# Performance work log

Hardware: AMD Instinct MI355X
Metric: run time of the kernel (lower is better)

Reference implementation:

```python
import jax, jax.numpy as jnp
import numpy as np

B, H, W, K, A = 4096, 32, 32, 20, 4


def setup_inputs() -> dict:
    key = jax.random.key(0)
    k_wall, k_agent, k_goal, k_phi, k_l1, k_l2 = jax.random.split(key, 6)
    # obs channels: 0 = wall/feature map (random), 1 = one-hot agent pos, 2 = one-hot goal pos
    walls = jax.random.uniform(k_wall, (B, H, W), dtype=jnp.float32)
    agent_idx = jax.random.randint(k_agent, (B,), 0, H * W)
    goal_idx = jax.random.randint(k_goal, (B,), 0, H * W)
    agent = jax.nn.one_hot(agent_idx, H * W, dtype=jnp.float32).reshape(B, H, W)
    goal = jax.nn.one_hot(goal_idx, H * W, dtype=jnp.float32).reshape(B, H, W)
    obs = jnp.stack([walls, agent, goal], axis=-1)  # (B,H,W,3)
    obs_flat = obs.reshape(B, H * W * 3)
    din = H * W * 3
    return {
        "obs_flat": obs_flat,
        "Phi_w": jax.random.normal(k_phi, (din, 2 * H * W), dtype=jnp.float32) * 0.02,
        "Phi_b": jnp.zeros((2 * H * W,), jnp.float32),
        "L1_w": jax.random.normal(k_l1, (36, 16), dtype=jnp.float32) * 0.1,
        "L1_b": jnp.zeros((16,), jnp.float32),
        "L2_w": jax.random.normal(k_l2, (16, A), dtype=jnp.float32) * 0.1,
        "L2_b": jnp.zeros((A,), jnp.float32),
    }


def _mvprop(r, p):
    # K-step value propagation: V <- max(V, r + p*(best 4-neighbor V - r))
    # p = sigmoid(...) >= 0, so max over the 4 shifted nv values equals nv of the max shift.
    def body(V, _):
        pv = jnp.pad(V, ((0, 0), (1, 1), (1, 1)))
        nbr = jnp.maximum(
            jnp.maximum(pv[:, :-2, 1:-1], pv[:, 2:, 1:-1]),   # up, down
            jnp.maximum(pv[:, 1:-1, :-2], pv[:, 1:-1, 2:]),   # left, right
        )
        return jnp.maximum(V, r + p * (nbr - r)), None
    V, _ = jax.lax.scan(body, r, None, length=K)
    return V


def reference(obs_flat, Phi_w, Phi_b, L1_w, L1_b, L2_w, L2_b):
    b = obs_flat.shape[0]
    obs = obs_flat.reshape(b, H, W, 3)
    phi = jax.nn.sigmoid(obs_flat @ Phi_w + Phi_b).reshape(b, H, W, 2)
    r, p = phi[..., 0], phi[..., 1]
    V = _mvprop(r, p)  # (b,H,W)
    obs_val = jnp.concatenate([obs, V[..., None]], axis=-1)  # (b,H,W,4)
    padded = jnp.pad(obs_val, ((0, 0), (1, 1), (1, 1), (0, 0)))
    # agent position: exactly one nonzero in channel 1 per sample -> argmax
    idx = jnp.argmax(obs[..., 1].reshape(b, -1), axis=1)
    pi, pj = idx // W, idx % W
    # 3x3 neighborhood around agent in padded grid (start = pos+1-1 = pos)
    def slice_one(ov, i, j):
        return jax.lax.dynamic_slice(ov, (i, j, 0), (3, 3, 4))
    sel = jax.vmap(slice_one)(padded, pi, pj)  # (b,3,3,4)
    h = jax.nn.relu(sel.reshape(b, 36) @ L1_w + L1_b)
    logit = h @ L2_w + L2_b
    return logit
```

## Files before the change

kernel.cpp:

```cpp
#include <hip/hip_runtime.h>
#include <hip/hip_fp16.h>

#define BATCH 4096
#define HH 32
#define WW 32
#define KPROP 20
#define NACT 4
#define DIN 3072
#define DPHI 2048
#define HWC 1024
#define KC 1024

typedef _Float16 h8_t __attribute__((ext_vector_type(8)));
typedef _Float16 h4_t __attribute__((ext_vector_type(4)));
typedef float f32x4 __attribute__((ext_vector_type(4)));

__device__ inline void load_lds16(const _Float16* g, _Float16* l) {
    __builtin_amdgcn_global_load_lds(
        (const __attribute__((address_space(1))) void*)g,
        (__attribute__((address_space(3))) void*)l, 16, 0, 0);
}

__device__ inline float sigmoidf(float x) { return 1.0f / (1.0f + __expf(-x)); }

__device__ inline float dpp_shr1(float x) {
    return __int_as_float(__builtin_amdgcn_update_dpp(
        0, __float_as_int(x), 0x111, 0xF, 0xF, true));
}
__device__ inline float dpp_shl1(float x) {
    return __int_as_float(__builtin_amdgcn_update_dpp(
        0, __float_as_int(x), 0x101, 0xF, 0xF, true));
}

__global__ __launch_bounds__(256) void prep_fused_kernel(
    const float* __restrict__ obs,
    const float* __restrict__ Phi_w,
    _Float16* __restrict__ W16,
    _Float16* __restrict__ PwT,
    _Float16* __restrict__ Pag,
    int* __restrict__ aidx, int* __restrict__ gidx)
{
    __shared__ float tile[32][33];
    if (blockIdx.x < BATCH) {
        const int t = blockIdx.x * 256 + threadIdx.x;
        const int b = t >> 8;
        const int c0 = (t & 255) * 4;
        const float* src = obs + (size_t)b * DIN + 3 * c0;
        const float4 f0 = *(const float4*)(src);
        const float4 f1 = *(const float4*)(src + 4);
        const float4 f2 = *(const float4*)(src + 8);
        h4_t w;
        w[0] = (_Float16)f0.x; w[1] = (_Float16)f0.w;
        w[2] = (_Float16)f1.z; w[3] = (_Float16)f2.y;
        *(h4_t*)(W16 + (size_t)b * KC + c0) = w;
        if (f0.y > 0.5f) aidx[b] = c0;
        if (f1.x > 0.5f) aidx[b] = c0 + 1;
        if (f1.w > 0.5f) aidx[b] = c0 + 2;
        if (f2.z > 0.5f) aidx[b] = c0 + 3;
        if (f0.z > 0.5f) gidx[b] = c0;
        if (f1.y > 0.5f) gidx[b] = c0 + 1;
        if (f2.x > 0.5f) gidx[b] = c0 + 2;
        if (f2.w > 0.5f) gidx[b] = c0 + 3;
    } else {
        const int bid = blockIdx.x - BATCH;
        const int ni = bid & 63;
        const int ci = bid >> 6;
        const int tx = threadIdx.x & 31;
        const int ty = threadIdx.x >> 5;
        #pragma unroll
        for (int s = 0; s < 4; s++) {
            const int r = ty + 8 * s;
            const int c = ci * 32 + r;
            const int n = ni * 32 + tx;
            tile[r][tx] = Phi_w[(size_t)(3 * c) * DPHI + n];
            Pag[(size_t)c * DPHI + n]         = (_Float16)Phi_w[(size_t)(3 * c + 1) * DPHI + n];
            Pag[(size_t)(HWC + c) * DPHI + n] = (_Float16)Phi_w[(size_t)(3 * c + 2) * DPHI + n];
        }
        __syncthreads();
        #pragma unroll
        for (int s = 0; s < 4; s++) {
            const int r = ty + 8 * s;
            PwT[(size_t)(ni * 32 + r) * KC + ci * 32 + tx] = (_Float16)tile[tx][r];
        }
    }
}

#define BM 64
#define BN 128

__device__ inline void stage_tile(const _Float16* Arow, const _Float16* Bbase, int k0,
                                  _Float16* As, _Float16* Bs, int tid) {
    load_lds16(Arow + k0, As + tid * 8);
    const int sk0 = tid >> 7;
    #pragma unroll
    for (int r2 = 0; r2 < 2; r2++) {
        const int kqs = sk0 + 2 * r2;
        load_lds16(Bbase + k0 + kqs * 8, Bs + (tid + 256 * r2) * 8);
    }
}

__global__ __launch_bounds__(256, 4) void gemm_pre_kernel(
    const _Float16* __restrict__ A,
    const _Float16* __restrict__ Bt,
    const float* __restrict__ bias,
    _Float16* __restrict__ pre)
{
    __shared__ _Float16 As[2][4 * BM * 8];
    __shared__ _Float16 Bs[2][4 * BN * 8];

    const int tid  = threadIdx.x;
    const int lane = tid & 63;
    const int wid  = tid >> 6;
    const int m0 = blockIdx.y * BM;
    const int n0 = blockIdx.x * BN;
    const int wm = (wid >> 1) * 32;
    const int wn = (wid & 1) * 64;
    const int lm = lane & 15;
    const int kq = lane >> 4;

    f32x4 acc[2][4] = {};

    const _Float16* Arow  = A  + (size_t)(m0 + (tid & 63)) * KC + (tid >> 6) * 8;
    const _Float16* Bbase = Bt + (size_t)(n0 + (tid & 127)) * KC;

    stage_tile(Arow, Bbase, 0, As[0], Bs[0], tid);

    int cur = 0;
    for (int k0 = 0; k0 < KC; k0 += 32) {
        __syncthreads();
        if (k0 + 32 < KC)
            stage_tile(Arow, Bbase, k0 + 32, As[cur ^ 1], Bs[cur ^ 1], tid);

        h8_t af[2], bf[4];
        #pragma unroll
        for (int mt = 0; mt < 2; mt++)
            af[mt] = *(const h8_t*)(As[cur] + (kq * BM + wm + mt * 16 + lm) * 8);
        #pragma unroll
        for (int nt = 0; nt < 4; nt++)
            bf[nt] = *(const h8_t*)(Bs[cur] + (kq * BN + wn + nt * 16 + lm) * 8);

        #pragma unroll
        for (int mt = 0; mt < 2; mt++)
            #pragma unroll
            for (int nt = 0; nt < 4; nt++)
                acc[mt][nt] = __builtin_amdgcn_mfma_f32_16x16x32_f16(
                    af[mt], bf[nt], acc[mt][nt], 0, 0, 0);
        cur ^= 1;
    }

    #pragma unroll
    for (int nt = 0; nt < 4; nt++) {
        const int col = n0 + wn + nt * 16 + lm;
        const float bcol = bias[col];
        #pragma unroll
        for (int mt = 0; mt < 2; mt++) {
            #pragma unroll
            for (int r = 0; r < 4; r++) {
                const int row = m0 + wm + mt * 16 + kq * 4 + r;
                pre[(size_t)row * DPHI + col] = (_Float16)(acc[mt][nt][r] + bcol);
            }
        }
    }
}

__global__ __launch_bounds__(256, 4) void vprop_head_kernel(
    const _Float16* __restrict__ pre,
    const _Float16* __restrict__ Pag,
    const float* __restrict__ obs,
    const int* __restrict__ aidx,
    const int* __restrict__ gidx,
    const float* __restrict__ L1w,
    const float* __restrict__ L1b,
    const float* __restrict__ L2w,
    const float* __restrict__ L2b,
    float* __restrict__ out)
{
    __shared__ __align__(16) float Vg[4][HWC];
    __shared__ float sel[4][36], hbuf[4][16];

    const int tid  = threadIdx.x;
    const int w    = tid >> 6;
    const int lane = tid & 63;
    const int b    = blockIdx.x * 4 + w;
    const int bi   = lane & 15;
    const int bj   = lane >> 4;
    const int ai = aidx[b];
    const int gi = gidx[b];

    const _Float16* pb = pre + (size_t)b * DPHI;
    const _Float16* ra = Pag + (size_t)ai * DPHI;
    const _Float16* rg = Pag + (size_t)(HWC + gi) * DPHI;

    float v[2][8], p[2][8], a[2][8];
    #pragma unroll
    for (int r = 0; r < 2; r++) {
        const int off = 64 * (2 * bi + r) + 16 * bj;
        const h8_t ph0 = *(const h8_t*)(pb + off), ph1 = *(const h8_t*)(pb + off + 8);
        const h8_t pa0 = *(const h8_t*)(ra + off), pa1 = *(const h8_t*)(ra + off + 8);
        const h8_t pg0 = *(const h8_t*)(rg + off), pg1 = *(const h8_t*)(rg + off + 8);
        #pragma unroll
        for (int c = 0; c < 4; c++) {
            const float rv = sigmoidf((float)ph0[2*c]   + (float)pa0[2*c]   + (float)pg0[2*c]);
            const float pv = sigmoidf((float)ph0[2*c+1] + (float)pa0[2*c+1] + (float)pg0[2*c+1]);
            v[r][c] = rv; p[r][c] = pv; a[r][c] = rv * (1.0f - pv);
            const float rv2 = sigmoidf((float)ph1[2*c]   + (float)pa1[2*c]   + (float)pg1[2*c]);
            const float pv2 = sigmoidf((float)ph1[2*c+1] + (float)pa1[2*c+1] + (float)pg1[2*c+1]);
            v[r][c+4] = rv2; p[r][c+4] = pv2; a[r][c+4] = rv2 * (1.0f - pv2);
        }
    }

    for (int it = 0; it < KPROP; it++) {
        float uh[8], dh[8], lh[2], rh[2];
        #pragma unroll
        for (int c = 0; c < 8; c++) {
            uh[c] = dpp_shr1(v[1][c]);
            dh[c] = dpp_shl1(v[0][c]);
        }
        #pragma unroll
        for (int r = 0; r < 2; r++) {
            lh[r] = __shfl(v[r][7], lane - 16);
            rh[r] = __shfl(v[r][0], lane + 16);
            if (bj == 0) lh[r] = 0.0f;
            if (bj == 3) rh[r] = 0.0f;
        }
        float nb[2][8];
        #pragma unroll
        for (int c = 0; c < 8; c++) {
            const float lf0 = (c == 0) ? lh[0] : v[0][c-1];
            const float rt0 = (c == 7) ? rh[0] : v[0][c+1];
            const float lf1 = (c == 0) ? lh[1] : v[1][c-1];
            const float rt1 = (c == 7) ? rh[1] : v[1][c+1];
            nb[0][c] = fmaxf(fmaxf(uh[c], v[1][c]), fmaxf(lf0, rt0));
            nb[1][c] = fmaxf(fmaxf(v[0][c], dh[c]), fmaxf(lf1, rt1));
        }
        #pragma unroll
        for (int r = 0; r < 2; r++)
            #pragma unroll
            for (int c = 0; c < 8; c++)
                v[r][c] = fmaxf(v[r][c], fmaf(p[r][c], nb[r][c], a[r][c]));
    }

    #pragma unroll
    for (int r = 0; r < 2; r++) {
        float4 lo, hi;
        lo.x = v[r][0]; lo.y = v[r][1]; lo.z = v[r][2]; lo.w = v[r][3];
        hi.x = v[r][4]; hi.y = v[r][5]; hi.z = v[r][6]; hi.w = v[r][7];
        const int base = (2 * bi + r) * 32 + 8 * bj;
        *(float4*)&Vg[w][base]     = lo;
        *(float4*)&Vg[w][base + 4] = hi;
    }
    __syncthreads();

    const int pi = ai >> 5, pj = ai & 31;
    if (lane < 36) {
        const int cell = lane >> 2;
        const int ch = lane & 3;
        const int di = pi + cell / 3 - 1;
        const int dj = pj + cell % 3 - 1;
        float vv = 0.0f;
        if (di >= 0 && di < HH && dj >= 0 && dj < WW) {
            const int c = di * WW + dj;
            vv = (ch < 3) ? obs[(size_t)b * DIN + 3 * c + ch] : Vg[w][c];
        }
        sel[w][lane] = vv;
    }
    __syncthreads();

    if (lane < 16) {
        float h = L1b[lane];
        #pragma unroll
        for (int k = 0; k < 36; k++) h += sel[w][k] * L1w[k * 16 + lane];
        hbuf[w][lane] = fmaxf(h, 0.0f);
    }
    __syncthreads();

    if (lane < 4) {
        float o = L2b[lane];
        #pragma unroll
        for (int t = 0; t < 16; t++) o += hbuf[w][t] * L2w[t * 4 + lane];
        out[(size_t)b * NACT + lane] = o;
    }
}

extern "C" void kernel_launch(void* const* d_in, const int* in_sizes, int n_in,
                              void* d_out, int out_size, void* d_ws, size_t ws_size,
                              hipStream_t stream) {
    const float* obs   = (const float*)d_in[0];
    const float* Phi_w = (const float*)d_in[1];
    const float* Phi_b = (const float*)d_in[2];
    const float* L1w   = (const float*)d_in[3];
    const float* L1b   = (const float*)d_in[4];
    const float* L2w   = (const float*)d_in[5];
    const float* L2b   = (const float*)d_in[6];
    float* out = (float*)d_out;

    char* ws = (char*)d_ws;
    _Float16* pre = (_Float16*)ws;
    _Float16* W16 = (_Float16*)(ws + 16777216);
    _Float16* PwT = (_Float16*)(ws + 25165824);
    _Float16* Pag = (_Float16*)(ws + 29360128);
    int* aidx = (int*)(ws + 37748736);
    int* gidx = aidx + BATCH;

    prep_fused_kernel<<<BATCH + 2048, 256, 0, stream>>>(obs, Phi_w, W16, PwT, Pag, aidx, gidx);
    gemm_pre_kernel<<<dim3(DPHI / BN, BATCH / BM), 256, 0, stream>>>(W16, PwT, Phi_b, pre);
    vprop_head_kernel<<<BATCH / 4, 256, 0, stream>>>(pre, Pag, obs, aidx, gidx,
                                                     L1w, L1b, L2w, L2b, out);
}
```

Before: 185.5 us.

## Replace LDS-staged GEMM with register double-buffered direct global loads

The Phi GEMM no longer stages A and B tiles through LDS with async global-to-LDS loads and barriers. Each wave instead loads its MFMA fragments straight from global memory into registers, prefetching the next k-slice. Each wave also computes a larger 64x64 output tile within a 64x256 block tile. This removes block-level synchronisation and LDS traffic, but it relies on caches for reuse of A across waves. It also uses strided, less coalesced global loads and raises register pressure.

```diff
diff --git a/kernel.cpp b/kernel.cpp
--- a/kernel.cpp
+++ b/kernel.cpp
@@ -14,12 +14,6 @@
 typedef _Float16 h8_t __attribute__((ext_vector_type(8)));
 typedef _Float16 h4_t __attribute__((ext_vector_type(4)));
 typedef float f32x4 __attribute__((ext_vector_type(4)));
-
-__device__ inline void load_lds16(const _Float16* g, _Float16* l) {
-    __builtin_amdgcn_global_load_lds(
-        (const __attribute__((address_space(1))) void*)g,
-        (__attribute__((address_space(3))) void*)l, 16, 0, 0);
-}
 
 __device__ inline float sigmoidf(float x) { return 1.0f / (1.0f + __expf(-x)); }
 
@@ -85,78 +79,59 @@
     }
 }
 
-#define BM 64
-#define BN 128
-
-__device__ inline void stage_tile(const _Float16* Arow, const _Float16* Bbase, int k0,
-                                  _Float16* As, _Float16* Bs, int tid) {
-    load_lds16(Arow + k0, As + tid * 8);
-    const int sk0 = tid >> 7;
-    #pragma unroll
-    for (int r2 = 0; r2 < 2; r2++) {
-        const int kqs = sk0 + 2 * r2;
-        load_lds16(Bbase + k0 + kqs * 8, Bs + (tid + 256 * r2) * 8);
-    }
-}
-
-__global__ __launch_bounds__(256, 4) void gemm_pre_kernel(
+__global__ __launch_bounds__(256) void gemm_pre_kernel(
     const _Float16* __restrict__ A,
     const _Float16* __restrict__ Bt,
     const float* __restrict__ bias,
     _Float16* __restrict__ pre)
 {
-    __shared__ _Float16 As[2][4 * BM * 8];
-    __shared__ _Float16 Bs[2][4 * BN * 8];
-
     const int tid  = threadIdx.x;
     const int lane = tid & 63;
     const int wid  = tid >> 6;
-    const int m0 = blockIdx.y * BM;
-    const int n0 = blockIdx.x * BN;
-    const int wm = (wid >> 1) * 32;
-    const int wn = (wid & 1) * 64;
+    const int m0 = blockIdx.y * 64;
+    const int n0 = blockIdx.x * 256 + wid * 64;
     const int lm = lane & 15;
     const int kq = lane >> 4;
 
-    f32x4 acc[2][4] = {};
-
-    const _Float16* Arow  = A  + (size_t)(m0 + (tid & 63)) * KC + (tid >> 6) * 8;
-    const _Float16* Bbase = Bt + (size_t)(n0 + (tid & 127)) * KC;
-
-    stage_tile(Arow, Bbase, 0, As[0], Bs[0], tid);
-
-    int cur = 0;
-    for (int k0 = 0; k0 < KC; k0 += 32) {
-        __syncthreads();
-        if (k0 + 32 < KC)
-            stage_tile(Arow, Bbase, k0 + 32, As[cur ^ 1], Bs[cur ^ 1], tid);
-
-        h8_t af[2], bf[4];
-        #pragma unroll
-        for (int mt = 0; mt < 2; mt++)
-            af[mt] = *(const h8_t*)(As[cur] + (kq * BM + wm + mt * 16 + lm) * 8);
-        #pragma unroll
-        for (int nt = 0; nt < 4; nt++)
-            bf[nt] = *(const h8_t*)(Bs[cur] + (kq * BN + wn + nt * 16 + lm) * 8);
-
-        #pragma unroll
-        for (int mt = 0; mt < 2; mt++)
+    const _Float16* Ap = A  + (size_t)(m0 + lm) * KC + kq * 8;
+    const _Float16* Bp = Bt + (size_t)(n0 + lm) * KC + kq * 8;
+
+    f32x4 acc[4][4] = {};
+    h8_t a_cur[4], b_cur[4], a_nxt[4], b_nxt[4];
+
+    #pragma unroll
+    for (int i = 0; i < 4; i++) {
+        a_cur[i] = *(const h8_t*)(Ap + (size_t)i * 16 * KC);
+        b_cur[i] = *(const h8_t*)(Bp + (size_t)i * 16 * KC);
+    }
+
+    for (int k0 = 32; k0 <= KC; k0 += 32) {
+        if (k0 < KC) {
+            #pragma unroll
+            for (int i = 0; i < 4; i++) {
+                a_nxt[i] = *(const h8_t*)(Ap + (size_t)i * 16 * KC + k0);
+                b_nxt[i] = *(const h8_t*)(Bp + (size_t)i * 16 * KC + k0);
+            }
+        }
+        #pragma unroll
+        for (int mt = 0; mt < 4; mt++)
             #pragma unroll
             for (int nt = 0; nt < 4; nt++)
                 acc[mt][nt] = __builtin_amdgcn_mfma_f32_16x16x32_f16(
-                    af[mt], bf[nt], acc[mt][nt], 0, 0, 0);
-        cur ^= 1;
+                    a_cur[mt], b_cur[nt], acc[mt][nt], 0, 0, 0);
+        #pragma unroll
+        for (int i = 0; i < 4; i++) { a_cur[i] = a_nxt[i]; b_cur[i] = b_nxt[i]; }
     }
 
     #pragma unroll
     for (int nt = 0; nt < 4; nt++) {
-        const int col = n0 + wn + nt * 16 + lm;
+        const int col = n0 + nt * 16 + lm;
         const float bcol = bias[col];
         #pragma unroll
-        for (int mt = 0; mt < 2; mt++) {
+        for (int mt = 0; mt < 4; mt++) {
             #pragma unroll
             for (int r = 0; r < 4; r++) {
-                const int row = m0 + wm + mt * 16 + kq * 4 + r;
+                const int row = m0 + mt * 16 + kq * 4 + r;
                 pre[(size_t)row * DPHI + col] = (_Float16)(acc[mt][nt][r] + bcol);
             }
         }
@@ -303,7 +278,7 @@
     int* gidx = aidx + BATCH;
 
     prep_fused_kernel<<<BATCH + 2048, 256, 0, stream>>>(obs, Phi_w, W16, PwT, Pag, aidx, gidx);
-    gemm_pre_kernel<<<dim3(DPHI / BN, BATCH / BM), 256, 0, stream>>>(W16, PwT, Phi_b, pre);
+    gemm_pre_kernel<<<dim3(DPHI / 256, BATCH / 64), 256, 0, stream>>>(W16, PwT, Phi_b, pre);
     vprop_head_kernel<<<BATCH / 4, 256, 0, stream>>>(pre, Pag, obs, aidx, gidx,
                                                      L1w, L1b, L2w, L2b, out);
 }
```

Result: slower. 197.2 us (+6.3%).
